# Kernel optimization log

Measured on AMD Instinct MI355X. Metric: run time of the kernel, lower is better.

## Reference

```python
import jax, jax.numpy as jnp
import numpy as np

N = 50000   # nodes
E = 409600  # edges
H = 2       # heads
C = 64      # per-head channels


def _seg_softmax(alpha, dst, n):
    # PyG-style softmax over edges grouped by destination node. alpha: [E, H]
    m = jax.ops.segment_max(alpha, dst, num_segments=n)
    m = jnp.where(jnp.isfinite(m), m, 0.0)
    ex = jnp.exp(alpha - m[dst])
    s = jax.ops.segment_sum(ex, dst, num_segments=n)
    return ex / (s[dst] + 1e-16)


def _tconv(x, src, dst, e, Wq, bq, Wk, bk, Wv, bv, We, Ws, bs, n):
    # PyG TransformerConv (concat=True, beta=False, root_weight=True, dropout=0)
    q = (x @ Wq + bq).reshape(n, H, C)
    k = (x @ Wk + bk).reshape(n, H, C)
    v = (x @ Wv + bv).reshape(n, H, C)
    eh = (e @ We).reshape(-1, H, C)          # lin_edge has no bias in PyG
    kj = k[src] + eh                          # [E, H, C]
    alpha = (q[dst] * kj).sum(-1) / jnp.sqrt(jnp.float32(C))  # [E, H]
    alpha = _seg_softmax(alpha, dst, n)
    msg = (v[src] + eh) * alpha[:, :, None]   # [E, H, C]
    out = jax.ops.segment_sum(msg, dst, num_segments=n).reshape(n, H * C)
    return out + x @ Ws + bs                  # root/skip connection


def setup_inputs() -> dict:
    key = jax.random.key(0)
    ks = jax.random.split(key, 32)

    def lin_w(k, i, o):
        return (jax.random.normal(k, (i, o), dtype=jnp.float32) / np.sqrt(i)).astype(jnp.float32)

    inp = {
        "x": jax.random.normal(ks[0], (N, 6), dtype=jnp.float32),
        "edge_index": jax.random.randint(ks[1], (2, E), 0, N, dtype=jnp.int32).astype(jnp.int64),
        "edge_attr": jax.random.normal(ks[2], (E, 1), dtype=jnp.float32),
        # edge encoder: Linear(1, 64)
        "We_enc": lin_w(ks[3], 1, 64), "be_enc": jnp.zeros((64,), jnp.float32),
        # conv1: TransformerConv(6, 64, heads=2, edge_dim=64)
        "Wq1": lin_w(ks[4], 6, H * C), "bq1": jnp.zeros((H * C,), jnp.float32),
        "Wk1": lin_w(ks[5], 6, H * C), "bk1": jnp.zeros((H * C,), jnp.float32),
        "Wv1": lin_w(ks[6], 6, H * C), "bv1": jnp.zeros((H * C,), jnp.float32),
        "We1": lin_w(ks[7], 64, H * C),
        "Ws1": lin_w(ks[8], 6, H * C), "bs1": jnp.zeros((H * C,), jnp.float32),
        # conv2: TransformerConv(128, 64, heads=2, edge_dim=64)
        "Wq2": lin_w(ks[9], 128, H * C), "bq2": jnp.zeros((H * C,), jnp.float32),
        "Wk2": lin_w(ks[10], 128, H * C), "bk2": jnp.zeros((H * C,), jnp.float32),
        "Wv2": lin_w(ks[11], 128, H * C), "bv2": jnp.zeros((H * C,), jnp.float32),
        "We2": lin_w(ks[12], 64, H * C),
        "Ws2": lin_w(ks[13], 128, H * C), "bs2": jnp.zeros((H * C,), jnp.float32),
        # fc: Linear(128, 1)
        "Wfc": lin_w(ks[14], 128, 1), "bfc": jnp.zeros((1,), jnp.float32),
    }
    return inp


def reference(x, edge_index, edge_attr,
              We_enc, be_enc,
              Wq1, bq1, Wk1, bk1, Wv1, bv1, We1, Ws1, bs1,
              Wq2, bq2, Wk2, bk2, Wv2, bv2, We2, Ws2, bs2,
              Wfc, bfc):
    src, dst = edge_index[0], edge_index[1]
    e = edge_attr @ We_enc + be_enc           # [E, 64]
    h = jax.nn.relu(_tconv(x, src, dst, e, Wq1, bq1, Wk1, bk1, Wv1, bv1, We1, Ws1, bs1, N))
    h = jax.nn.relu(_tconv(h, src, dst, e, Wq2, bq2, Wk2, bk2, Wv2, bv2, We2, Ws2, bs2, N))
    return h @ Wfc + bfc                      # [N, 1]
```

## Files before the change

kernel.cpp:

```cpp
#include <hip/hip_runtime.h>


#define HC 128

typedef __attribute__((ext_vector_type(8))) short bf16x8;
typedef __attribute__((ext_vector_type(4))) float f32x4;

__device__ __forceinline__ unsigned bf16_rne(float f) {
    unsigned u = __float_as_uint(f);
    return (u + 0x7fffu + ((u >> 16) & 1u)) >> 16;
}

__global__ void k_uc(const float* __restrict__ We_enc, const float* __restrict__ be_enc,
                     const float* __restrict__ We1, const float* __restrict__ We2,
                     float* __restrict__ uc) {
    int c = threadIdx.x;
    float u1 = 0.f, c1 = 0.f, u2 = 0.f, c2 = 0.f;
    for (int j = 0; j < 64; ++j) {
        float we = We_enc[j], be = be_enc[j];
        float w1 = We1[j * HC + c], w2 = We2[j * HC + c];
        u1 += we * w1; c1 += be * w1;
        u2 += we * w2; c2 += be * w2;
    }
    uc[c] = u1; uc[HC + c] = c1; uc[2 * HC + c] = u2; uc[3 * HC + c] = c2;
}

__global__ __launch_bounds__(256) void k_wpack(
    const float* __restrict__ Wq, const float* __restrict__ Wk,
    const float* __restrict__ Wv, const float* __restrict__ Ws,
    unsigned short* __restrict__ Bph) {
    int t = blockIdx.x * 256 + threadIdx.x;
    int nn = t >> 7;
    int kk = t & 127;
    int mat = nn >> 7, c = nn & 127;
    const float* W = (mat == 0) ? Wq : (mat == 1) ? Wk : (mat == 2) ? Wv : Ws;
    Bph[nn * 128 + kk] = (unsigned short)bf16_rne(W[kk * 128 + c]);
}

__global__ __launch_bounds__(256) void k_hist(const int* __restrict__ ei, int* __restrict__ deg, int E) {
    int t = blockIdx.x * blockDim.x + threadIdx.x;
    if (t < E) atomicAdd(&deg[ei[E + t]], 1);
}

__global__ __launch_bounds__(256) void k_scan1(const int* __restrict__ deg, int* __restrict__ bsum, int n) {
    int t = blockIdx.x * 256 + threadIdx.x;
    int v = (t < n) ? deg[t] : 0;
#pragma unroll
    for (int off = 1; off < 64; off <<= 1) v += __shfl_xor(v, off);
    __shared__ int wsum[4];
    int lane = threadIdx.x & 63, w = threadIdx.x >> 6;
    if (lane == 0) wsum[w] = v;
    __syncthreads();
    if (threadIdx.x == 0) bsum[blockIdx.x] = wsum[0] + wsum[1] + wsum[2] + wsum[3];
}

__global__ __launch_bounds__(256) void k_scan2(int* __restrict__ bsum, int nb) {
    __shared__ int sh[256];
    int t = threadIdx.x;
    int v = (t < nb) ? bsum[t] : 0;
    sh[t] = v;
    __syncthreads();
    for (int off = 1; off < 256; off <<= 1) {
        int x = (t >= off) ? sh[t - off] : 0;
        __syncthreads();
        sh[t] += x;
        __syncthreads();
    }
    if (t < nb) bsum[t] = sh[t] - v;
}

__global__ __launch_bounds__(256) void k_scan3(const int* __restrict__ deg, const int* __restrict__ bsum,
                                               int* __restrict__ rowptr, int n, int E) {
    int t = blockIdx.x * 256 + threadIdx.x;
    int tid = threadIdx.x;
    int v = (t < n) ? deg[t] : 0;
    __shared__ int sh[256];
    sh[tid] = v;
    __syncthreads();
    for (int off = 1; off < 256; off <<= 1) {
        int x = (tid >= off) ? sh[tid - off] : 0;
        __syncthreads();
        sh[tid] += x;
        __syncthreads();
    }
    if (t < n) rowptr[t] = bsum[blockIdx.x] + sh[tid] - v;
    if (t == 0) rowptr[n] = E;
}

__global__ __launch_bounds__(256) void k_scatter(const int* __restrict__ ei, const int* __restrict__ rowptr,
                                                 int* __restrict__ cursor, int* __restrict__ eid, int E) {
    int t = blockIdx.x * blockDim.x + threadIdx.x;
    if (t >= E) return;
    int dst = ei[E + t];
    int pos = rowptr[dst] + atomicAdd(&cursor[dst], 1);
    eid[pos] = t;
}

__global__ __launch_bounds__(256) void k_bsort(const int* __restrict__ rowptr, int* __restrict__ eid, int n) {
    int t = blockIdx.x * blockDim.x + threadIdx.x;
    if (t >= n) return;
    int b = rowptr[t], e = rowptr[t + 1];
    for (int i = b + 1; i < e; ++i) {
        int key = eid[i];
        int j = i - 1;
        while (j >= b && eid[j] > key) { eid[j + 1] = eid[j]; --j; }
        eid[j + 1] = key;
    }
}

__global__ __launch_bounds__(256) void k_gather(const int* __restrict__ eid, const int* __restrict__ ei,
                                                const float* __restrict__ ea,
                                                int* __restrict__ srcs, float* __restrict__ eas, int E) {
    int t = blockIdx.x * blockDim.x + threadIdx.x;
    if (t >= E) return;
    int id = eid[t];
    srcs[t] = ei[id];
    eas[t] = ea[id];
}

__global__ __launch_bounds__(256) void k_lin6(
    const float* __restrict__ X, int n,
    const float* __restrict__ Wq, const float* __restrict__ bq,
    const float* __restrict__ Wk, const float* __restrict__ bk,
    const float* __restrict__ Wv, const float* __restrict__ bv,
    const float* __restrict__ Ws, const float* __restrict__ bs,
    float* __restrict__ q, unsigned short* __restrict__ kv,
    float* __restrict__ o) {
    __shared__ float xs[16][6];
    const int base = blockIdx.x * 16;
    const int tid = threadIdx.x;
    for (int i = tid; i < 16 * 6; i += 256) {
        int ni = base + i / 6;
        xs[i / 6][i % 6] = (ni < n) ? X[(size_t)ni * 6 + (i % 6)] : 0.f;
    }
    __syncthreads();
    const int c = tid & 127;
    const int m = tid >> 7;
    const float* WA = m ? Wv : Wq;
    const float* WB = m ? Ws : Wk;
    float accA[16], accB[16];
#pragma unroll
    for (int i = 0; i < 16; ++i) { accA[i] = 0.f; accB[i] = 0.f; }
    for (int j = 0; j < 6; ++j) {
        float w0 = WA[j * HC + c];
        float w1 = WB[j * HC + c];
#pragma unroll
        for (int i = 0; i < 16; ++i) {
            float xv = xs[i][j];
            accA[i] += xv * w0;
            accB[i] += xv * w1;
        }
    }
    if (m == 0) {
        const float bA = bq[c], bB = bk[c];
#pragma unroll
        for (int i = 0; i < 16; ++i) {
            int ni = base + i;
            if (ni < n) {
                q[(size_t)ni * HC + c] = accA[i] + bA;
                kv[(size_t)ni * 256 + c] = (unsigned short)bf16_rne(accB[i] + bB);
            }
        }
    } else {
        const float bA = bv[c], bB = bs[c];
#pragma unroll
        for (int i = 0; i < 16; ++i) {
            int ni = base + i;
            if (ni < n) {
                kv[(size_t)ni * 256 + 128 + c] = (unsigned short)bf16_rne(accA[i] + bA);
                o[(size_t)ni * HC + c] = accB[i] + bB;
            }
        }
    }
}

__global__ __launch_bounds__(256, 4) void k_lin2(
    const unsigned short* __restrict__ hb, const unsigned short* __restrict__ Bph,
    const float* __restrict__ bq, const float* __restrict__ bk,
    const float* __restrict__ bv, const float* __restrict__ bs,
    float* __restrict__ q, unsigned short* __restrict__ kv,
    float* __restrict__ o, int n) {
    __shared__ unsigned short Bs[128][128];
    const int tid = threadIdx.x;
    const int wid = tid >> 6, l = tid & 63;
    const int la = l & 15, lk = l >> 4;
    const int mb = blockIdx.x * 64;
    int nodeA = mb + wid * 16 + la;
    if (nodeA >= n) nodeA = n - 1;
    const int sw = (la & 7) << 3;
    const int crow0 = mb + wid * 16 + lk * 4;

    bf16x8 areg[4];
#pragma unroll
    for (int ks = 0; ks < 4; ++ks)
        areg[ks] = *(const bf16x8*)&hb[(size_t)nodeA * 128 + lk * 8 + ks * 32];

    for (int cq = 0; cq < 4; ++cq) {
        if (cq) __syncthreads();
        for (int i = tid; i < 128 * 16; i += 256) {
            int kk8 = i & 15;
            int nnl = i >> 4;
            bf16x8 val = *(const bf16x8*)&Bph[((size_t)(cq * 128 + nnl)) * 128 + kk8 * 8];
            int swk = (kk8 ^ (nnl & 7)) * 8;
            *(bf16x8*)&Bs[nnl][swk] = val;
        }
        __syncthreads();

        f32x4 acc[8];
#pragma unroll
        for (int nt = 0; nt < 8; ++nt) acc[nt] = (f32x4){0.f, 0.f, 0.f, 0.f};
#pragma unroll
        for (int ks = 0; ks < 4; ++ks) {
            const int rk = (lk * 8 + ks * 32) ^ sw;
#pragma unroll
            for (int nt = 0; nt < 8; ++nt) {
                bf16x8 Bh = *(const bf16x8*)&Bs[nt * 16 + la][rk];
                acc[nt] = __builtin_amdgcn_mfma_f32_16x16x32_bf16(areg[ks], Bh, acc[nt], 0, 0, 0);
            }
        }
        const float* bias = (cq == 0) ? bq : (cq == 1) ? bk : (cq == 2) ? bv : bs;
#pragma unroll
        for (int nt = 0; nt < 8; ++nt) {
            const int col = nt * 16 + la;
            const float bb = bias[col];
            if (cq == 0 || cq == 3) {
                float* out = (cq == 0) ? q : o;
#pragma unroll
                for (int j = 0; j < 4; ++j) {
                    int n0 = crow0 + j;
                    if (n0 < n) out[(size_t)n0 * 128 + col] = acc[nt][j] + bb;
                }
            } else {
                const int co = (cq == 1) ? col : 128 + col;
#pragma unroll
                for (int j = 0; j < 4; ++j) {
                    int n0 = crow0 + j;
                    if (n0 < n) kv[(size_t)n0 * 256 + co] = (unsigned short)bf16_rne(acc[nt][j] + bb);
                }
            }
        }
    }
}

template <int MODE>
__global__ __launch_bounds__(256) void k_attn(
    const float* __restrict__ q, const unsigned short* __restrict__ kvp,
    const int* __restrict__ rowptr, const int* __restrict__ srcs, const float* __restrict__ eas,
    const float* __restrict__ ucu, const float* __restrict__ ucc,
    float* __restrict__ io, unsigned short* __restrict__ hb, int n) {
    int wid = (int)((blockIdx.x * (size_t)blockDim.x + threadIdx.x) >> 6);
    int lane = threadIdx.x & 63;
    if (wid >= n) return;
    const int half = lane >> 5;
    const int hl = lane & 31;
    const int ch = hl * 4;

    float4 qr = *(const float4*)&q[(size_t)wid * 128 + ch];
    float4 uu = *(const float4*)&ucu[ch];
    float4 cc = *(const float4*)&ucc[ch];

    float qu = qr.x * uu.x + qr.y * uu.y + qr.z * uu.z + qr.w * uu.w;
    float qc = qr.x * cc.x + qr.y * cc.y + qr.z * cc.z + qr.w * cc.w;
#pragma unroll
    for (int off = 1; off < 16; off <<= 1) {
        qu += __shfl_xor(qu, off);
        qc += __shfl_xor(qc, off);
    }

    int b = rowptr[wid], e = rowptr[wid + 1];
    float m = -3.0e38f, s = 0.f, sea = 0.f;
    float av0 = 0.f, av1 = 0.f, av2 = 0.f, av3 = 0.f;

    if (b < e) {
        int pi = b + half;
        bool val = pi < e;
        int pc = val ? pi : e - 1;
        int src = srcs[pc];
        float eav = eas[pc];
        const unsigned short* row = &kvp[(size_t)src * 256 + ch];
        uint2 ku = *(const uint2*)row;
        uint2 vu = *(const uint2*)(row + 128);
        for (int p = b; p < e; p += 2) {
            int pn = p + 2 + half;
            bool valn = pn < e;
            int pcn = valn ? pn : e - 1;
            int srcn = srcs[pcn];
            float eavn = eas[pcn];
            const unsigned short* rown = &kvp[(size_t)srcn * 256 + ch];
            uint2 kun = *(const uint2*)rown;
            uint2 vun = *(const uint2*)(rown + 128);

            float k0 = __uint_as_float(ku.x << 16);
            float k1 = __uint_as_float(ku.x & 0xffff0000u);
            float k2 = __uint_as_float(ku.y << 16);
            float k3 = __uint_as_float(ku.y & 0xffff0000u);
            float d = qr.x * k0 + qr.y * k1 + qr.z * k2 + qr.w * k3;
#pragma unroll
            for (int off = 1; off < 16; off <<= 1) d += __shfl_xor(d, off);
            float a = val ? (d + fmaf(eav, qu, qc)) * 0.125f : -INFINITY;
            float nm = fmaxf(m, a);
            float sc = __expf(m - nm);
            float pw = __expf(a - nm);
            float v0 = __uint_as_float(vu.x << 16);
            float v1 = __uint_as_float(vu.x & 0xffff0000u);
            float v2 = __uint_as_float(vu.y << 16);
            float v3 = __uint_as_float(vu.y & 0xffff0000u);
            s = fmaf(s, sc, pw);
            sea = fmaf(sea, sc, pw * eav);
            av0 = fmaf(av0, sc, pw * v0);
            av1 = fmaf(av1, sc, pw * v1);
            av2 = fmaf(av2, sc, pw * v2);
            av3 = fmaf(av3, sc, pw * v3);
            m = nm;
            ku = kun; vu = vun; eav = eavn; val = valn;
        }
    }

    {
        float om = __shfl_xor(m, 32);
        float os = __shfl_xor(s, 32);
        float osea = __shfl_xor(sea, 32);
        float o0 = __shfl_xor(av0, 32);
        float o1 = __shfl_xor(av1, 32);
        float o2 = __shfl_xor(av2, 32);
        float o3 = __shfl_xor(av3, 32);
        float nm = fmaxf(m, om);
        float scS = __expf(m - nm);
        float scO = __expf(om - nm);
        s = s * scS + os * scO;
        sea = sea * scS + osea * scO;
        av0 = av0 * scS + o0 * scO;
        av1 = av1 * scS + o1 * scO;
        av2 = av2 * scS + o2 * scO;
        av3 = av3 * scS + o3 * scO;
    }

    if (half == 0) {
        float inv = 1.f / (s + 1e-16f);
        float4 skip = *(const float4*)&io[(size_t)wid * 128 + ch];
        float r0 = (av0 + uu.x * sea + cc.x * s) * inv + skip.x;
        float r1 = (av1 + uu.y * sea + cc.y * s) * inv + skip.y;
        float r2 = (av2 + uu.z * sea + cc.z * s) * inv + skip.z;
        float r3 = (av3 + uu.w * sea + cc.w * s) * inv + skip.w;
        if (MODE == 1) {
            r0 = fmaxf(r0, 0.f); r1 = fmaxf(r1, 0.f);
            r2 = fmaxf(r2, 0.f); r3 = fmaxf(r3, 0.f);
            ushort4 hv = make_ushort4((unsigned short)bf16_rne(r0),
                                      (unsigned short)bf16_rne(r1),
                                      (unsigned short)bf16_rne(r2),
                                      (unsigned short)bf16_rne(r3));
            *(ushort4*)&hb[(size_t)wid * 128 + ch] = hv;
        } else {
            *(float4*)&io[(size_t)wid * 128 + ch] = make_float4(r0, r1, r2, r3);
        }
    }
}

__global__ __launch_bounds__(256) void k_fc(
    const float* __restrict__ h, const float* __restrict__ Wfc,
    const float* __restrict__ bfc, float* __restrict__ out, int n) {
    int w = (int)((blockIdx.x * (size_t)blockDim.x + threadIdx.x) >> 6);
    int lane = threadIdx.x & 63;
    if (w >= n) return;
    const float2* h2 = (const float2*)h;
    const float2* w2 = (const float2*)Wfc;
    float2 hv = h2[(size_t)w * 64 + lane];
    float2 wv = w2[lane];
    float vsum = fmaxf(hv.x, 0.f) * wv.x + fmaxf(hv.y, 0.f) * wv.y;
#pragma unroll
    for (int off = 1; off < 64; off <<= 1) vsum += __shfl_xor(vsum, off);
    if (lane == 0) out[w] = vsum + bfc[0];
}

extern "C" void kernel_launch(void* const* d_in, const int* in_sizes, int n_in,
                              void* d_out, int out_size, void* d_ws, size_t ws_size,
                              hipStream_t stream) {
    const float* x      = (const float*)d_in[0];
    const int*   ei     = (const int*)d_in[1];
    const float* ea     = (const float*)d_in[2];
    const float* We_enc = (const float*)d_in[3];
    const float* be_enc = (const float*)d_in[4];
    const float* Wq1 = (const float*)d_in[5],  *bq1 = (const float*)d_in[6];
    const float* Wk1 = (const float*)d_in[7],  *bk1 = (const float*)d_in[8];
    const float* Wv1 = (const float*)d_in[9],  *bv1 = (const float*)d_in[10];
    const float* We1 = (const float*)d_in[11];
    const float* Ws1 = (const float*)d_in[12], *bs1 = (const float*)d_in[13];
    const float* Wq2 = (const float*)d_in[14], *bq2 = (const float*)d_in[15];
    const float* Wk2 = (const float*)d_in[16], *bk2 = (const float*)d_in[17];
    const float* Wv2 = (const float*)d_in[18], *bv2 = (const float*)d_in[19];
    const float* We2 = (const float*)d_in[20];
    const float* Ws2 = (const float*)d_in[21], *bs2 = (const float*)d_in[22];
    const float* Wfc = (const float*)d_in[23], *bfc = (const float*)d_in[24];

    const int n = in_sizes[0] / 6;
    const int E = in_sizes[2];

    float* ws = (float*)d_ws;
    size_t off = 0;
    float* qb = ws + off; off += (size_t)n * HC;
    float* Bb = ws + off; off += (size_t)n * HC;
    unsigned short* kv16 = (unsigned short*)(ws + off); off += (size_t)n * HC;
    int* rowptr = (int*)(ws + off); off += (size_t)(n + 1);
    int* deg    = (int*)(ws + off); off += (size_t)n;
    int* bsum   = (int*)(ws + off); off += 256;
    int* eid    = (int*)(ws + off); off += (size_t)E;
    int* srcs   = (int*)(ws + off); off += (size_t)E;
    float* eas  = ws + off; off += (size_t)E;
    float* uc   = ws + off; off += 512;
    unsigned short* hb16 = (unsigned short*)(ws + off); off += (size_t)n * HC / 2;
    unsigned short* Bph = (unsigned short*)(ws + off); off += 512 * 128 / 2;

    const int eb = (E + 255) / 256;
    const int nb = (n + 255) / 256;
    const int wb = (int)(((size_t)n * 64 + 255) / 256);

    hipLaunchKernelGGL(k_uc, dim3(1), dim3(128), 0, stream, We_enc, be_enc, We1, We2, uc);
    hipLaunchKernelGGL(k_wpack, dim3(256), dim3(256), 0, stream, Wq2, Wk2, Wv2, Ws2, Bph);

    hipMemsetAsync(deg, 0, (size_t)n * sizeof(int), stream);
    hipLaunchKernelGGL(k_hist, dim3(eb), dim3(256), 0, stream, ei, deg, E);
    hipLaunchKernelGGL(k_scan1, dim3(nb), dim3(256), 0, stream, deg, bsum, n);
    hipLaunchKernelGGL(k_scan2, dim3(1), dim3(256), 0, stream, bsum, nb);
    hipLaunchKernelGGL(k_scan3, dim3(nb), dim3(256), 0, stream, deg, bsum, rowptr, n, E);
    hipMemsetAsync(deg, 0, (size_t)n * sizeof(int), stream);
    hipLaunchKernelGGL(k_scatter, dim3(eb), dim3(256), 0, stream, ei, rowptr, deg, eid, E);
    hipLaunchKernelGGL(k_bsort, dim3(nb), dim3(256), 0, stream, rowptr, eid, n);
    hipLaunchKernelGGL(k_gather, dim3(eb), dim3(256), 0, stream, eid, ei, ea, srcs, eas, E);

    hipLaunchKernelGGL(k_lin6, dim3((n + 15) / 16), dim3(256), 0, stream,
                       x, n, Wq1, bq1, Wk1, bk1, Wv1, bv1, Ws1, bs1, qb, kv16, Bb);
    hipLaunchKernelGGL((k_attn<1>), dim3(wb), dim3(256), 0, stream,
                       qb, kv16, rowptr, srcs, eas, uc, uc + HC, Bb, hb16, n);

    hipLaunchKernelGGL(k_lin2, dim3((n + 63) / 64), dim3(256), 0, stream,
                       hb16, Bph, bq2, bk2, bv2, bs2, qb, kv16, Bb, n);
    hipLaunchKernelGGL((k_attn<0>), dim3(wb), dim3(256), 0, stream,
                       qb, kv16, rowptr, srcs, eas, uc + 2 * HC, uc + 3 * HC, Bb,
                       (unsigned short*)nullptr, n);

    hipLaunchKernelGGL(k_fc, dim3(wb), dim3(256), 0, stream, Bb, Wfc, bfc, (float*)d_out, n);
}
```

Measured before the change: 231.7 us.

## Fuse gather into sort, fc into attention, dual-stream attention accumulators

Several changes land together. The second memset of deg moves into k_scan3, the separate gather kernel is merged into the per-node insertion sort, and the final fc projection is folded into the layer-2 attention kernel so the layer-2 output is no longer written to and re-read from memory. The attention loop now processes four edges per iteration with two independent online-softmax accumulator sets, to expose more memory-level parallelism across the irregular gathers. The costs are more registers per thread and a serial, uncoalesced gather loop inside the sort kernel, which runs one thread per node.

```diff
diff --git a/kernel.cpp b/kernel.cpp
--- a/kernel.cpp
+++ b/kernel.cpp
@@ -69,7 +69,7 @@
     if (t < nb) bsum[t] = sh[t] - v;
 }
 
-__global__ __launch_bounds__(256) void k_scan3(const int* __restrict__ deg, const int* __restrict__ bsum,
+__global__ __launch_bounds__(256) void k_scan3(int* __restrict__ deg, const int* __restrict__ bsum,
                                                int* __restrict__ rowptr, int n, int E) {
     int t = blockIdx.x * 256 + threadIdx.x;
     int tid = threadIdx.x;
@@ -83,7 +83,7 @@
         sh[tid] += x;
         __syncthreads();
     }
-    if (t < n) rowptr[t] = bsum[blockIdx.x] + sh[tid] - v;
+    if (t < n) { rowptr[t] = bsum[blockIdx.x] + sh[tid] - v; deg[t] = 0; }
     if (t == 0) rowptr[n] = E;
 }
 
@@ -96,7 +96,10 @@
     eid[pos] = t;
 }
 
-__global__ __launch_bounds__(256) void k_bsort(const int* __restrict__ rowptr, int* __restrict__ eid, int n) {
+__global__ __launch_bounds__(256) void k_bsortg(
+    const int* __restrict__ rowptr, int* __restrict__ eid,
+    const int* __restrict__ ei, const float* __restrict__ ea,
+    int* __restrict__ srcs, float* __restrict__ eas, int n) {
     int t = blockIdx.x * blockDim.x + threadIdx.x;
     if (t >= n) return;
     int b = rowptr[t], e = rowptr[t + 1];
@@ -106,16 +109,11 @@
         while (j >= b && eid[j] > key) { eid[j + 1] = eid[j]; --j; }
         eid[j + 1] = key;
     }
-}
-
-__global__ __launch_bounds__(256) void k_gather(const int* __restrict__ eid, const int* __restrict__ ei,
-                                                const float* __restrict__ ea,
-                                                int* __restrict__ srcs, float* __restrict__ eas, int E) {
-    int t = blockIdx.x * blockDim.x + threadIdx.x;
-    if (t >= E) return;
-    int id = eid[t];
-    srcs[t] = ei[id];
-    eas[t] = ea[id];
+    for (int i = b; i < e; ++i) {
+        int id = eid[i];
+        srcs[i] = ei[id];
+        eas[i] = ea[id];
+    }
 }
 
 __global__ __launch_bounds__(256) void k_lin6(
@@ -242,12 +240,40 @@
     }
 }
 
+#define UPD(mS, sS, seaS, a0S, a1S, a2S, a3S, kuS, vuS, eaS, vS)          \
+    do {                                                                  \
+        float k0 = __uint_as_float((kuS).x << 16);                        \
+        float k1 = __uint_as_float((kuS).x & 0xffff0000u);                \
+        float k2 = __uint_as_float((kuS).y << 16);                        \
+        float k3 = __uint_as_float((kuS).y & 0xffff0000u);                \
+        float d = qr.x * k0 + qr.y * k1 + qr.z * k2 + qr.w * k3;          \
+        d += __shfl_xor(d, 1); d += __shfl_xor(d, 2);                     \
+        d += __shfl_xor(d, 4); d += __shfl_xor(d, 8);                     \
+        float a = (vS) ? (d + fmaf(eaS, qu, qc)) * 0.125f : -INFINITY;    \
+        float nm = fmaxf(mS, a);                                          \
+        float sc = __expf(mS - nm);                                       \
+        float pw = __expf(a - nm);                                        \
+        float v0 = __uint_as_float((vuS).x << 16);                        \
+        float v1 = __uint_as_float((vuS).x & 0xffff0000u);                \
+        float v2 = __uint_as_float((vuS).y << 16);                        \
+        float v3 = __uint_as_float((vuS).y & 0xffff0000u);                \
+        sS = fmaf(sS, sc, pw);                                            \
+        seaS = fmaf(seaS, sc, pw * (eaS));                                \
+        a0S = fmaf(a0S, sc, pw * v0);                                     \
+        a1S = fmaf(a1S, sc, pw * v1);                                     \
+        a2S = fmaf(a2S, sc, pw * v2);                                     \
+        a3S = fmaf(a3S, sc, pw * v3);                                     \
+        mS = nm;                                                          \
+    } while (0)
+
 template <int MODE>
 __global__ __launch_bounds__(256) void k_attn(
     const float* __restrict__ q, const unsigned short* __restrict__ kvp,
     const int* __restrict__ rowptr, const int* __restrict__ srcs, const float* __restrict__ eas,
     const float* __restrict__ ucu, const float* __restrict__ ucc,
-    float* __restrict__ io, unsigned short* __restrict__ hb, int n) {
+    const float* __restrict__ io, unsigned short* __restrict__ hb,
+    const float* __restrict__ Wfc, const float* __restrict__ bfc,
+    float* __restrict__ out, int n) {
     int wid = (int)((blockIdx.x * (size_t)blockDim.x + threadIdx.x) >> 6);
     int lane = threadIdx.x & 63;
     if (wid >= n) return;
@@ -268,108 +294,91 @@
     }
 
     int b = rowptr[wid], e = rowptr[wid + 1];
-    float m = -3.0e38f, s = 0.f, sea = 0.f;
-    float av0 = 0.f, av1 = 0.f, av2 = 0.f, av3 = 0.f;
+    float mX = -3.0e38f, sX = 0.f, seaX = 0.f, aX0 = 0.f, aX1 = 0.f, aX2 = 0.f, aX3 = 0.f;
+    float mY = -3.0e38f, sY = 0.f, seaY = 0.f, aY0 = 0.f, aY1 = 0.f, aY2 = 0.f, aY3 = 0.f;
 
     if (b < e) {
-        int pi = b + half;
-        bool val = pi < e;
-        int pc = val ? pi : e - 1;
-        int src = srcs[pc];
-        float eav = eas[pc];
-        const unsigned short* row = &kvp[(size_t)src * 256 + ch];
-        uint2 ku = *(const uint2*)row;
-        uint2 vu = *(const uint2*)(row + 128);
-        for (int p = b; p < e; p += 2) {
-            int pn = p + 2 + half;
-            bool valn = pn < e;
-            int pcn = valn ? pn : e - 1;
-            int srcn = srcs[pcn];
-            float eavn = eas[pcn];
-            const unsigned short* rown = &kvp[(size_t)srcn * 256 + ch];
-            uint2 kun = *(const uint2*)rown;
-            uint2 vun = *(const uint2*)(rown + 128);
-
-            float k0 = __uint_as_float(ku.x << 16);
-            float k1 = __uint_as_float(ku.x & 0xffff0000u);
-            float k2 = __uint_as_float(ku.y << 16);
-            float k3 = __uint_as_float(ku.y & 0xffff0000u);
-            float d = qr.x * k0 + qr.y * k1 + qr.z * k2 + qr.w * k3;
-#pragma unroll
-            for (int off = 1; off < 16; off <<= 1) d += __shfl_xor(d, off);
-            float a = val ? (d + fmaf(eav, qu, qc)) * 0.125f : -INFINITY;
-            float nm = fmaxf(m, a);
-            float sc = __expf(m - nm);
-            float pw = __expf(a - nm);
-            float v0 = __uint_as_float(vu.x << 16);
-            float v1 = __uint_as_float(vu.x & 0xffff0000u);
-            float v2 = __uint_as_float(vu.y << 16);
-            float v3 = __uint_as_float(vu.y & 0xffff0000u);
-            s = fmaf(s, sc, pw);
-            sea = fmaf(sea, sc, pw * eav);
-            av0 = fmaf(av0, sc, pw * v0);
-            av1 = fmaf(av1, sc, pw * v1);
-            av2 = fmaf(av2, sc, pw * v2);
-            av3 = fmaf(av3, sc, pw * v3);
-            m = nm;
-            ku = kun; vu = vun; eav = eavn; val = valn;
+        int pX = b + half;       bool vX = pX < e; int cX = vX ? pX : e - 1;
+        int pY = b + 2 + half;   bool vY = pY < e; int cY = vY ? pY : e - 1;
+        int sx = srcs[cX], sy = srcs[cY];
+        float eaX = eas[cX], eaY = eas[cY];
+        const unsigned short* rX = &kvp[(size_t)sx * 256 + ch];
+        const unsigned short* rY = &kvp[(size_t)sy * 256 + ch];
+        uint2 kuX = *(const uint2*)rX, vuX = *(const uint2*)(rX + 128);
+        uint2 kuY = *(const uint2*)rY, vuY = *(const uint2*)(rY + 128);
+        for (int p = b; p < e; p += 4) {
+            int pXn = p + 4 + half;  bool vXn = pXn < e; int cXn = vXn ? pXn : e - 1;
+            int pYn = p + 6 + half;  bool vYn = pYn < e; int cYn = vYn ? pYn : e - 1;
+            int sxn = srcs[cXn], syn = srcs[cYn];
+            float eaXn = eas[cXn], eaYn = eas[cYn];
+            const unsigned short* rXn = &kvp[(size_t)sxn * 256 + ch];
+            const unsigned short* rYn = &kvp[(size_t)syn * 256 + ch];
+            uint2 kuXn = *(const uint2*)rXn, vuXn = *(const uint2*)(rXn + 128);
+            uint2 kuYn = *(const uint2*)rYn, vuYn = *(const uint2*)(rYn + 128);
+
+            UPD(mX, sX, seaX, aX0, aX1, aX2, aX3, kuX, vuX, eaX, vX);
+            UPD(mY, sY, seaY, aY0, aY1, aY2, aY3, kuY, vuY, eaY, vY);
+
+            kuX = kuXn; vuX = vuXn; eaX = eaXn; vX = vXn;
+            kuY = kuYn; vuY = vuYn; eaY = eaYn; vY = vYn;
         }
     }
 
     {
-        float om = __shfl_xor(m, 32);
-        float os = __shfl_xor(s, 32);
-        float osea = __shfl_xor(sea, 32);
-        float o0 = __shfl_xor(av0, 32);
-        float o1 = __shfl_xor(av1, 32);
-        float o2 = __shfl_xor(av2, 32);
-        float o3 = __shfl_xor(av3, 32);
-        float nm = fmaxf(m, om);
-        float scS = __expf(m - nm);
+        float nm = fmaxf(mX, mY);
+        float scX = __expf(mX - nm);
+        float scY = __expf(mY - nm);
+        sX = sX * scX + sY * scY;
+        seaX = seaX * scX + seaY * scY;
+        aX0 = aX0 * scX + aY0 * scY;
+        aX1 = aX1 * scX + aY1 * scY;
+        aX2 = aX2 * scX + aY2 * scY;
+        aX3 = aX3 * scX + aY3 * scY;
+        mX = nm;
+    }
+    {
+        float om = __shfl_xor(mX, 32);
+        float os = __shfl_xor(sX, 32);
+        float osea = __shfl_xor(seaX, 32);
+        float o0 = __shfl_xor(aX0, 32);
+        float o1 = __shfl_xor(aX1, 32);
+        float o2 = __shfl_xor(aX2, 32);
+        float o3 = __shfl_xor(aX3, 32);
+        float nm = fmaxf(mX, om);
+        float scS = __expf(mX - nm);
         float scO = __expf(om - nm);
-        s = s * scS + os * scO;
-        sea = sea * scS + osea * scO;
-        av0 = av0 * scS + o0 * scO;
-        av1 = av1 * scS + o1 * scO;
-        av2 = av2 * scS + o2 * scO;
-        av3 = av3 * scS + o3 * scO;
-    }
-
-    if (half == 0) {
-        float inv = 1.f / (s + 1e-16f);
-        float4 skip = *(const float4*)&io[(size_t)wid * 128 + ch];
-        float r0 = (av0 + uu.x * sea + cc.x * s) * inv + skip.x;
-        float r1 = (av1 + uu.y * sea + cc.y * s) * inv + skip.y;
-        float r2 = (av2 + uu.z * sea + cc.z * s) * inv + skip.z;
-        float r3 = (av3 + uu.w * sea + cc.w * s) * inv + skip.w;
-        if (MODE == 1) {
-            r0 = fmaxf(r0, 0.f); r1 = fmaxf(r1, 0.f);
-            r2 = fmaxf(r2, 0.f); r3 = fmaxf(r3, 0.f);
+        sX = sX * scS + os * scO;
+        seaX = seaX * scS + osea * scO;
+        aX0 = aX0 * scS + o0 * scO;
+        aX1 = aX1 * scS + o1 * scO;
+        aX2 = aX2 * scS + o2 * scO;
+        aX3 = aX3 * scS + o3 * scO;
+    }
+
+    float inv = 1.f / (sX + 1e-16f);
+    float4 skip = *(const float4*)&io[(size_t)wid * 128 + ch];
+    float r0 = (aX0 + uu.x * seaX + cc.x * sX) * inv + skip.x;
+    float r1 = (aX1 + uu.y * seaX + cc.y * sX) * inv + skip.y;
+    float r2 = (aX2 + uu.z * seaX + cc.z * sX) * inv + skip.z;
+    float r3 = (aX3 + uu.w * seaX + cc.w * sX) * inv + skip.w;
+    r0 = fmaxf(r0, 0.f); r1 = fmaxf(r1, 0.f);
+    r2 = fmaxf(r2, 0.f); r3 = fmaxf(r3, 0.f);
+
+    if (MODE == 1) {
+        if (half == 0) {
             ushort4 hv = make_ushort4((unsigned short)bf16_rne(r0),
                                       (unsigned short)bf16_rne(r1),
                                       (unsigned short)bf16_rne(r2),
                                       (unsigned short)bf16_rne(r3));
             *(ushort4*)&hb[(size_t)wid * 128 + ch] = hv;
-        } else {
-            *(float4*)&io[(size_t)wid * 128 + ch] = make_float4(r0, r1, r2, r3);
-        }
-    }
-}
-
-__global__ __launch_bounds__(256) void k_fc(
-    const float* __restrict__ h, const float* __restrict__ Wfc,
-    const float* __restrict__ bfc, float* __restrict__ out, int n) {
-    int w = (int)((blockIdx.x * (size_t)blockDim.x + threadIdx.x) >> 6);
-    int lane = threadIdx.x & 63;
-    if (w >= n) return;
-    const float2* h2 = (const float2*)h;
-    const float2* w2 = (const float2*)Wfc;
-    float2 hv = h2[(size_t)w * 64 + lane];
-    float2 wv = w2[lane];
-    float vsum = fmaxf(hv.x, 0.f) * wv.x + fmaxf(hv.y, 0.f) * wv.y;
-#pragma unroll
-    for (int off = 1; off < 64; off <<= 1) vsum += __shfl_xor(vsum, off);
-    if (lane == 0) out[w] = vsum + bfc[0];
+        }
+    } else {
+        float4 wf = *(const float4*)&Wfc[ch];
+        float rr = r0 * wf.x + r1 * wf.y + r2 * wf.z + r3 * wf.w;
+#pragma unroll
+        for (int off = 1; off < 32; off <<= 1) rr += __shfl_xor(rr, off);
+        if (lane == 0) out[wid] = rr + bfc[0];
+    }
 }
 
 extern "C" void kernel_launch(void* const* d_in, const int* in_sizes, int n_in,
@@ -422,21 +431,18 @@
     hipLaunchKernelGGL(k_scan1, dim3(nb), dim3(256), 0, stream, deg, bsum, n);
     hipLaunchKernelGGL(k_scan2, dim3(1), dim3(256), 0, stream, bsum, nb);
     hipLaunchKernelGGL(k_scan3, dim3(nb), dim3(256), 0, stream, deg, bsum, rowptr, n, E);
-    hipMemsetAsync(deg, 0, (size_t)n * sizeof(int), stream);
     hipLaunchKernelGGL(k_scatter, dim3(eb), dim3(256), 0, stream, ei, rowptr, deg, eid, E);
-    hipLaunchKernelGGL(k_bsort, dim3(nb), dim3(256), 0, stream, rowptr, eid, n);
-    hipLaunchKernelGGL(k_gather, dim3(eb), dim3(256), 0, stream, eid, ei, ea, srcs, eas, E);
+    hipLaunchKernelGGL(k_bsortg, dim3(nb), dim3(256), 0, stream, rowptr, eid, ei, ea, srcs, eas, n);
 
     hipLaunchKernelGGL(k_lin6, dim3((n + 15) / 16), dim3(256), 0, stream,
                        x, n, Wq1, bq1, Wk1, bk1, Wv1, bv1, Ws1, bs1, qb, kv16, Bb);
     hipLaunchKernelGGL((k_attn<1>), dim3(wb), dim3(256), 0, stream,
-                       qb, kv16, rowptr, srcs, eas, uc, uc + HC, Bb, hb16, n);
+                       qb, kv16, rowptr, srcs, eas, uc, uc + HC, Bb, hb16,
+                       Wfc, bfc, (float*)d_out, n);
 
     hipLaunchKernelGGL(k_lin2, dim3((n + 63) / 64), dim3(256), 0, stream,
                        hb16, Bph, bq2, bk2, bv2, bs2, qb, kv16, Bb, n);
     hipLaunchKernelGGL((k_attn<0>), dim3(wb), dim3(256), 0, stream,
                        qb, kv16, rowptr, srcs, eas, uc + 2 * HC, uc + 3 * HC, Bb,
-                       (unsigned short*)nullptr, n);
-
-    hipLaunchKernelGGL(k_fc, dim3(wb), dim3(256), 0, stream, Bb, Wfc, bfc, (float*)d_out, n);
-}
+                       (unsigned short*)nullptr, Wfc, bfc, (float*)d_out, n);
+}
```

Result: faster. 227.2 us (-2.0%).
